# Kernel tuning notes

Measured on AMD Instinct MI355X. Metric: run time of the kernel, lower is better.

Reference implementation:

```python
import jax, jax.numpy as jnp
import numpy as np

D_MODEL = 1024
NUM_HEADS = 16
D_K = D_MODEL // NUM_HEADS


def setup_inputs() -> dict:
    key = jax.random.key(0)
    ks = jax.random.split(key, 9)
    s = 1.0 / np.sqrt(D_MODEL)
    inp = {
        "x": jax.random.normal(ks[0], (4, 2048, D_MODEL), dtype=jnp.float32),
        "W_q": jax.random.uniform(ks[1], (D_MODEL, D_MODEL), jnp.float32, -s, s),
        "b_q": jax.random.uniform(ks[2], (D_MODEL,), jnp.float32, -s, s),
        "W_k": jax.random.uniform(ks[3], (D_MODEL, D_MODEL), jnp.float32, -s, s),
        "b_k": jax.random.uniform(ks[4], (D_MODEL,), jnp.float32, -s, s),
        "W_v": jax.random.uniform(ks[5], (D_MODEL, D_MODEL), jnp.float32, -s, s),
        "b_v": jax.random.uniform(ks[6], (D_MODEL,), jnp.float32, -s, s),
        "W_o": jax.random.uniform(ks[7], (D_MODEL, D_MODEL), jnp.float32, -s, s),
        "b_o": jax.random.uniform(ks[8], (D_MODEL,), jnp.float32, -s, s),
    }
    return inp


def reference(x, W_q, b_q, W_k, b_k, W_v, b_v, W_o, b_o):
    B, S, _ = x.shape
    # Linear layers (torch convention: y = x @ W.T + b), split into heads -> [B, H, S, d_k]
    def proj(W, b):
        y = jnp.einsum("bsd,ed->bse", x, W) + b
        return y.reshape(B, S, NUM_HEADS, D_K).transpose(0, 2, 1, 3)

    Q = proj(W_q, b_q)
    K = proj(W_k, b_k)
    V = proj(W_v, b_v)

    scale = 1.0 / jnp.sqrt(jnp.asarray(D_K, dtype=x.dtype))
    scores = jnp.einsum("bhqd,bhkd->bhqk", Q, K) * scale  # [B, H, S, S]
    attn = jax.nn.softmax(scores, axis=-1)
    out = jnp.einsum("bhqk,bhkd->bhqd", attn, V)  # [B, H, S, d_k]
    out = out.transpose(0, 2, 1, 3).reshape(B, S, D_MODEL)
    return jnp.einsum("bsd,ed->bse", out, W_o) + b_o
```

## Files before the change

kernel.cpp:

```cpp
#include <hip/hip_runtime.h>
#include <math.h>


constexpr int D = 1024;
constexpr int H = 16;
constexpr int DK = 64;

typedef unsigned short u16;
typedef __attribute__((ext_vector_type(8))) short v8s;
typedef __attribute__((ext_vector_type(4))) float v4f;
typedef const __attribute__((address_space(1))) void gvoid;
typedef __attribute__((address_space(3))) void lvoid;

__device__ __forceinline__ u16 rne_bf16(float f) {
  unsigned u = __float_as_uint(f);
  u += 0x7FFFu + ((u >> 16) & 1u);
  return (u16)(u >> 16);
}

__global__ __launch_bounds__(256) void split_kernel(
    const float* __restrict__ in, u16* __restrict__ hi, u16* __restrict__ lo, int n4)
{
  const int i = blockIdx.x * 256 + threadIdx.x;
  if (i >= n4) return;
  const float4 v = ((const float4*)in)[i];
  const float f[4] = {v.x, v.y, v.z, v.w};
  ushort4 h, l;
  u16 hh[4], ll[4];
#pragma unroll
  for (int j = 0; j < 4; ++j) {
    const unsigned u = __float_as_uint(f[j]);
    hh[j] = (u16)(u >> 16);
    const float hf = __uint_as_float(u & 0xFFFF0000u);
    ll[j] = rne_bf16(f[j] - hf);
  }
  h.x = hh[0]; h.y = hh[1]; h.z = hh[2]; h.w = hh[3];
  l.x = ll[0]; l.y = ll[1]; l.z = ll[2]; l.w = ll[3];
  ((ushort4*)hi)[i] = h;
  ((ushort4*)lo)[i] = l;
}

__global__ __launch_bounds__(256) void gemm_mfma_kernel(
    const u16* __restrict__ Ahi, const u16* __restrict__ Alo,
    const u16* __restrict__ Whi, const u16* __restrict__ Wlo,
    const float* __restrict__ bias, void* __restrict__ Cout,
    int M, int S_, int headsplit_in, int out_mode)
{
  __shared__ u16 sAhi[128 * 32];
  __shared__ u16 sAlo[128 * 32];
  __shared__ u16 sBhi[128 * 32];
  __shared__ u16 sBlo[128 * 32];

  const int tid = threadIdx.x;
  const int m0 = blockIdx.x * 128, n0 = blockIdx.y * 128;
  const int lane = tid & 63, w = tid >> 6;
  const int wm = (w >> 1) * 64, wn = (w & 1) * 64;
  const int fr = lane & 15, fq = lane >> 4;

  v4f acc[4][4];
#pragma unroll
  for (int mi = 0; mi < 4; ++mi)
#pragma unroll
    for (int ni = 0; ni < 4; ++ni)
      acc[mi][ni] = (v4f){0.f, 0.f, 0.f, 0.f};

  const int srow = tid >> 2;
  const int skel = (tid & 3) * 8;

  for (int k0 = 0; k0 < D; k0 += 32) {
#pragma unroll
    for (int rep = 0; rep < 2; ++rep) {
      const int row = srow + rep * 64;
      size_t offA;
      if (headsplit_in) {
        const int m = m0 + row;
        const int b = m / S_, s = m - b * S_;
        const int k = k0 + skel;
        const int h = k >> 6, dk = k & 63;
        offA = ((size_t)(b * H + h) * S_ + s) * DK + dk;
      } else {
        offA = (size_t)(m0 + row) * D + k0 + skel;
      }
      const size_t offB = (size_t)(n0 + row) * D + k0 + skel;
      const int ldso = rep * 2048 + tid * 8;
      __builtin_amdgcn_global_load_lds((gvoid*)(Ahi + offA), (lvoid*)(sAhi + ldso), 16, 0, 0);
      __builtin_amdgcn_global_load_lds((gvoid*)(Alo + offA), (lvoid*)(sAlo + ldso), 16, 0, 0);
      __builtin_amdgcn_global_load_lds((gvoid*)(Whi + offB), (lvoid*)(sBhi + ldso), 16, 0, 0);
      __builtin_amdgcn_global_load_lds((gvoid*)(Wlo + offB), (lvoid*)(sBlo + ldso), 16, 0, 0);
    }
    __syncthreads();

    v8s ahi[4], alo[4], bhi[4], blo[4];
#pragma unroll
    for (int t = 0; t < 4; ++t) {
      const int ar = (wm + t * 16 + fr) * 32 + fq * 8;
      const int br = (wn + t * 16 + fr) * 32 + fq * 8;
      ahi[t] = *(const v8s*)&sAhi[ar];
      alo[t] = *(const v8s*)&sAlo[ar];
      bhi[t] = *(const v8s*)&sBhi[br];
      blo[t] = *(const v8s*)&sBlo[br];
    }
#pragma unroll
    for (int mi = 0; mi < 4; ++mi)
#pragma unroll
      for (int ni = 0; ni < 4; ++ni) {
        acc[mi][ni] = __builtin_amdgcn_mfma_f32_16x16x32_bf16(ahi[mi], bhi[ni], acc[mi][ni], 0, 0, 0);
        acc[mi][ni] = __builtin_amdgcn_mfma_f32_16x16x32_bf16(alo[mi], bhi[ni], acc[mi][ni], 0, 0, 0);
        acc[mi][ni] = __builtin_amdgcn_mfma_f32_16x16x32_bf16(ahi[mi], blo[ni], acc[mi][ni], 0, 0, 0);
      }
    __syncthreads();
  }

  float* Cf = (float*)Cout;
  u16* Cb = (u16*)Cout;
#pragma unroll
  for (int mi = 0; mi < 4; ++mi) {
#pragma unroll
    for (int ni = 0; ni < 4; ++ni) {
      const int n = n0 + wn + ni * 16 + fr;
      const float bv = bias[n];
#pragma unroll
      for (int r = 0; r < 4; ++r) {
        const int m = m0 + wm + mi * 16 + fq * 4 + r;
        const float val = acc[mi][ni][r] + bv;
        if (out_mode == 0) {
          Cf[(size_t)m * D + n] = val;
        } else {
          const int b = m / S_, s = m - b * S_;
          const int h = n >> 6, dk = n & 63;
          if (out_mode == 1)
            Cb[((size_t)(b * H + h) * S_ + s) * DK + dk] = rne_bf16(val);
          else
            Cb[((size_t)(b * H + h) * DK + dk) * S_ + s] = rne_bf16(val);
        }
      }
    }
  }
}

__global__ __launch_bounds__(256) void attn_mfma_kernel(
    const u16* __restrict__ Qb, const u16* __restrict__ Kb, const u16* __restrict__ Vtb,
    u16* __restrict__ Ohi, u16* __restrict__ Olo, int S_)
{
  __shared__ u16 Ks[64 * 64];
  __shared__ u16 Vt[64 * 64];
  __shared__ u16 Pl[4][32 * 72];

  const int tid = threadIdx.x;
  const int lane = tid & 63, w = tid >> 6;
  const int fr = lane & 15, fq = lane >> 4;
  const int q0 = blockIdx.x * 128;
  const int wq = w * 32;
  const size_t base = (size_t)(blockIdx.z * H + blockIdx.y) * S_ * DK;

  const int srow = tid >> 3;
  const int scb = (tid & 7) ^ (srow & 7);

  v8s qa[2][2];
#pragma unroll
  for (int mi = 0; mi < 2; ++mi)
#pragma unroll
    for (int ks = 0; ks < 2; ++ks)
      qa[mi][ks] = *(const v8s*)(Qb + base + (size_t)(q0 + wq + mi * 16 + fr) * DK + ks * 32 + fq * 8);

  v4f o[2][4];
  float lsum[2][4];
#pragma unroll
  for (int mi = 0; mi < 2; ++mi) {
#pragma unroll
    for (int ni = 0; ni < 4; ++ni) o[mi][ni] = (v4f){0.f, 0.f, 0.f, 0.f};
#pragma unroll
    for (int r = 0; r < 4; ++r) lsum[mi][r] = 0.f;
  }

  for (int j0 = 0; j0 < S_; j0 += 64) {
    __syncthreads();
#pragma unroll
    for (int rep = 0; rep < 2; ++rep) {
      const int row = rep * 32 + srow;
      const int ldso = rep * 2048 + tid * 8;
      __builtin_amdgcn_global_load_lds((gvoid*)(Kb + base + (size_t)(j0 + row) * DK + scb * 8),
                                       (lvoid*)(Ks + ldso), 16, 0, 0);
      __builtin_amdgcn_global_load_lds((gvoid*)(Vtb + base + (size_t)row * S_ + j0 + scb * 8),
                                       (lvoid*)(Vt + ldso), 16, 0, 0);
    }
    __syncthreads();

    v4f s[2][4];
#pragma unroll
    for (int mi = 0; mi < 2; ++mi)
#pragma unroll
      for (int ni = 0; ni < 4; ++ni) s[mi][ni] = (v4f){0.f, 0.f, 0.f, 0.f};
#pragma unroll
    for (int ks = 0; ks < 2; ++ks) {
      v8s kb[4];
#pragma unroll
      for (int ni = 0; ni < 4; ++ni) {
        const int row = ni * 16 + fr;
        kb[ni] = *(const v8s*)&Ks[row * 64 + (((ks * 4 + fq) ^ (row & 7)) * 8)];
      }
#pragma unroll
      for (int mi = 0; mi < 2; ++mi)
#pragma unroll
        for (int ni = 0; ni < 4; ++ni)
          s[mi][ni] = __builtin_amdgcn_mfma_f32_16x16x32_bf16(qa[mi][ks], kb[ni], s[mi][ni], 0, 0, 0);
    }

#pragma unroll
    for (int mi = 0; mi < 2; ++mi)
#pragma unroll
      for (int ni = 0; ni < 4; ++ni) {
#pragma unroll
        for (int r = 0; r < 4; ++r) {
          const float p = __expf(s[mi][ni][r] * 0.125f);
          s[mi][ni][r] = p;
          lsum[mi][r] += p;
          Pl[w][(mi * 16 + fq * 4 + r) * 72 + ni * 16 + fr] = rne_bf16(p);
        }
      }

#pragma unroll
    for (int ks = 0; ks < 2; ++ks) {
      v8s pa[2], vb[4];
#pragma unroll
      for (int mi = 0; mi < 2; ++mi)
        pa[mi] = *(const v8s*)&Pl[w][(mi * 16 + fr) * 72 + ks * 32 + fq * 8];
#pragma unroll
      for (int ni = 0; ni < 4; ++ni) {
        const int row = ni * 16 + fr;
        vb[ni] = *(const v8s*)&Vt[row * 64 + (((ks * 4 + fq) ^ (row & 7)) * 8)];
      }
#pragma unroll
      for (int mi = 0; mi < 2; ++mi)
#pragma unroll
        for (int ni = 0; ni < 4; ++ni)
          o[mi][ni] = __builtin_amdgcn_mfma_f32_16x16x32_bf16(pa[mi], vb[ni], o[mi][ni], 0, 0, 0);
    }
  }

#pragma unroll
  for (int mi = 0; mi < 2; ++mi)
#pragma unroll
    for (int r = 0; r < 4; ++r) {
#pragma unroll
      for (int off = 1; off < 16; off <<= 1)
        lsum[mi][r] += __shfl_xor(lsum[mi][r], off, 16);
      lsum[mi][r] = 1.f / lsum[mi][r];
    }

#pragma unroll
  for (int mi = 0; mi < 2; ++mi)
#pragma unroll
    for (int ni = 0; ni < 4; ++ni)
#pragma unroll
      for (int r = 0; r < 4; ++r) {
        const float val = o[mi][ni][r] * lsum[mi][r];
        const size_t addr = base + (size_t)(q0 + wq + mi * 16 + fq * 4 + r) * DK + ni * 16 + fr;
        const unsigned u = __float_as_uint(val);
        const u16 hv = (u16)(u >> 16);
        Ohi[addr] = hv;
        Olo[addr] = rne_bf16(val - __uint_as_float(u & 0xFFFF0000u));
      }
}

extern "C" void kernel_launch(void* const* d_in, const int* in_sizes, int n_in,
                              void* d_out, int out_size, void* d_ws, size_t ws_size,
                              hipStream_t stream) {
  const float* x  = (const float*)d_in[0];
  const float* Wq = (const float*)d_in[1];
  const float* bq = (const float*)d_in[2];
  const float* Wk = (const float*)d_in[3];
  const float* bk = (const float*)d_in[4];
  const float* Wv = (const float*)d_in[5];
  const float* bv = (const float*)d_in[6];
  const float* Wo = (const float*)d_in[7];
  const float* bo = (const float*)d_in[8];

  const int M = in_sizes[0] / D;
  const int B = 4;
  const int S_ = M / B;
  const size_t MD = (size_t)M * D;
  const size_t DD = (size_t)D * D;

  u16* Qb    = (u16*)d_ws;
  u16* Kb    = Qb + MD;
  u16* Vtb   = Kb + MD;
  u16* xs_hi = Vtb + MD;
  u16* xs_lo = xs_hi + MD;
  u16* wo_hi = xs_lo + MD;
  u16* wo_lo = wo_hi + DD;

  u16* wq_hi = (u16*)d_out;
  u16* wq_lo = wq_hi + DD;
  u16* wk_hi = wq_lo + DD;
  u16* wk_lo = wk_hi + DD;
  u16* wv_hi = wk_lo + DD;
  u16* wv_lo = wv_hi + DD;

  const int gx = (int)(MD / 4 / 256);
  const int gw = (int)(DD / 4 / 256);

  split_kernel<<<gx, 256, 0, stream>>>(x,  xs_hi, xs_lo, (int)(MD / 4));
  split_kernel<<<gw, 256, 0, stream>>>(Wq, wq_hi, wq_lo, (int)(DD / 4));
  split_kernel<<<gw, 256, 0, stream>>>(Wk, wk_hi, wk_lo, (int)(DD / 4));
  split_kernel<<<gw, 256, 0, stream>>>(Wv, wv_hi, wv_lo, (int)(DD / 4));
  split_kernel<<<gw, 256, 0, stream>>>(Wo, wo_hi, wo_lo, (int)(DD / 4));

  dim3 g(M / 128, D / 128);
  gemm_mfma_kernel<<<g, 256, 0, stream>>>(xs_hi, xs_lo, wq_hi, wq_lo, bq, Qb,  M, S_, 0, 1);
  gemm_mfma_kernel<<<g, 256, 0, stream>>>(xs_hi, xs_lo, wk_hi, wk_lo, bk, Kb,  M, S_, 0, 1);
  gemm_mfma_kernel<<<g, 256, 0, stream>>>(xs_hi, xs_lo, wv_hi, wv_lo, bv, Vtb, M, S_, 0, 2);

  dim3 ga(S_ / 128, H, B);
  attn_mfma_kernel<<<ga, 256, 0, stream>>>(Qb, Kb, Vtb, xs_hi, xs_lo, S_);

  gemm_mfma_kernel<<<g, 256, 0, stream>>>(xs_hi, xs_lo, wo_hi, wo_lo, bo, d_out, M, S_, 1, 0);
}
```

Baseline: 454.6 us.

## Fuse QKV projections into one GEMM launch and transpose attention MFMA layout

Concatenates the split Q/K/V weights into one buffer so a single GEMM launch computes all three projections, selecting bias and output layout per block column. The attention kernel swaps MFMA operand order so each lane holds a query column, which allows packed bf16 stores of P and vectorised output writes. Attention output is written directly in [B,S,D] token-major layout into separate buffers, so the output GEMM no longer needs head-split address math. This trades extra workspace for fewer launches, better tail occupancy and more coalesced stores.

```diff
diff --git a/kernel.cpp b/kernel.cpp
--- a/kernel.cpp
+++ b/kernel.cpp
@@ -1,10 +1,12 @@
 #include <hip/hip_runtime.h>
+#include <hip/hip_bf16.h>
 #include <math.h>
 
 
 constexpr int D = 1024;
 constexpr int H = 16;
 constexpr int DK = 64;
+constexpr int PSTR = 72;
 
 typedef unsigned short u16;
 typedef __attribute__((ext_vector_type(8))) short v8s;
@@ -16,6 +18,11 @@
   unsigned u = __float_as_uint(f);
   u += 0x7FFFu + ((u >> 16) & 1u);
   return (u16)(u >> 16);
+}
+
+__device__ __forceinline__ unsigned pk_bf16(float a, float b) {
+  __hip_bfloat162 t = __float22bfloat162_rn(float2{a, b});
+  return *reinterpret_cast<unsigned*>(&t);
 }
 
 __global__ __launch_bounds__(256) void split_kernel(
@@ -40,30 +47,18 @@
   ((ushort4*)lo)[i] = l;
 }
 
-__global__ __launch_bounds__(256) void gemm_mfma_kernel(
+struct GemmAcc { v4f a[4][4]; };
+
+__device__ __forceinline__ void gemm_body(
     const u16* __restrict__ Ahi, const u16* __restrict__ Alo,
     const u16* __restrict__ Whi, const u16* __restrict__ Wlo,
-    const float* __restrict__ bias, void* __restrict__ Cout,
-    int M, int S_, int headsplit_in, int out_mode)
-{
-  __shared__ u16 sAhi[128 * 32];
-  __shared__ u16 sAlo[128 * 32];
-  __shared__ u16 sBhi[128 * 32];
-  __shared__ u16 sBlo[128 * 32];
-
+    int m0, int nrow0, GemmAcc& g,
+    u16* sAhi, u16* sAlo, u16* sBhi, u16* sBlo)
+{
   const int tid = threadIdx.x;
-  const int m0 = blockIdx.x * 128, n0 = blockIdx.y * 128;
   const int lane = tid & 63, w = tid >> 6;
   const int wm = (w >> 1) * 64, wn = (w & 1) * 64;
   const int fr = lane & 15, fq = lane >> 4;
-
-  v4f acc[4][4];
-#pragma unroll
-  for (int mi = 0; mi < 4; ++mi)
-#pragma unroll
-    for (int ni = 0; ni < 4; ++ni)
-      acc[mi][ni] = (v4f){0.f, 0.f, 0.f, 0.f};
-
   const int srow = tid >> 2;
   const int skel = (tid & 3) * 8;
 
@@ -71,17 +66,8 @@
 #pragma unroll
     for (int rep = 0; rep < 2; ++rep) {
       const int row = srow + rep * 64;
-      size_t offA;
-      if (headsplit_in) {
-        const int m = m0 + row;
-        const int b = m / S_, s = m - b * S_;
-        const int k = k0 + skel;
-        const int h = k >> 6, dk = k & 63;
-        offA = ((size_t)(b * H + h) * S_ + s) * DK + dk;
-      } else {
-        offA = (size_t)(m0 + row) * D + k0 + skel;
-      }
-      const size_t offB = (size_t)(n0 + row) * D + k0 + skel;
+      const size_t offA = (size_t)(m0 + row) * D + k0 + skel;
+      const size_t offB = (size_t)(nrow0 + row) * D + k0 + skel;
       const int ldso = rep * 2048 + tid * 8;
       __builtin_amdgcn_global_load_lds((gvoid*)(Ahi + offA), (lvoid*)(sAhi + ldso), 16, 0, 0);
       __builtin_amdgcn_global_load_lds((gvoid*)(Alo + offA), (lvoid*)(sAlo + ldso), 16, 0, 0);
@@ -104,38 +90,102 @@
     for (int mi = 0; mi < 4; ++mi)
 #pragma unroll
       for (int ni = 0; ni < 4; ++ni) {
-        acc[mi][ni] = __builtin_amdgcn_mfma_f32_16x16x32_bf16(ahi[mi], bhi[ni], acc[mi][ni], 0, 0, 0);
-        acc[mi][ni] = __builtin_amdgcn_mfma_f32_16x16x32_bf16(alo[mi], bhi[ni], acc[mi][ni], 0, 0, 0);
-        acc[mi][ni] = __builtin_amdgcn_mfma_f32_16x16x32_bf16(ahi[mi], blo[ni], acc[mi][ni], 0, 0, 0);
+        g.a[mi][ni] = __builtin_amdgcn_mfma_f32_16x16x32_bf16(ahi[mi], bhi[ni], g.a[mi][ni], 0, 0, 0);
+        g.a[mi][ni] = __builtin_amdgcn_mfma_f32_16x16x32_bf16(alo[mi], bhi[ni], g.a[mi][ni], 0, 0, 0);
+        g.a[mi][ni] = __builtin_amdgcn_mfma_f32_16x16x32_bf16(ahi[mi], blo[ni], g.a[mi][ni], 0, 0, 0);
       }
     __syncthreads();
   }
-
-  float* Cf = (float*)Cout;
-  u16* Cb = (u16*)Cout;
+}
+
+__global__ __launch_bounds__(256) void gemm_qkv_kernel(
+    const u16* __restrict__ Ahi, const u16* __restrict__ Alo,
+    const u16* __restrict__ Whi, const u16* __restrict__ Wlo,
+    const float* __restrict__ bq, const float* __restrict__ bk, const float* __restrict__ bv,
+    u16* __restrict__ Qb, u16* __restrict__ Kb, u16* __restrict__ Vtb,
+    int S_)
+{
+  __shared__ u16 sAhi[128 * 32];
+  __shared__ u16 sAlo[128 * 32];
+  __shared__ u16 sBhi[128 * 32];
+  __shared__ u16 sBlo[128 * 32];
+
+  GemmAcc g;
+#pragma unroll
+  for (int mi = 0; mi < 4; ++mi)
+#pragma unroll
+    for (int ni = 0; ni < 4; ++ni) g.a[mi][ni] = (v4f){0.f, 0.f, 0.f, 0.f};
+
+  const int m0 = blockIdx.x * 128;
+  gemm_body(Ahi, Alo, Whi, Wlo, m0, blockIdx.y * 128, g, sAhi, sAlo, sBhi, sBlo);
+
+  const int wsel = blockIdx.y >> 3;
+  const float* bias = (wsel == 0) ? bq : (wsel == 1) ? bk : bv;
+  u16* Cb = (wsel == 0) ? Qb : (wsel == 1) ? Kb : Vtb;
+  const int n0l = (blockIdx.y & 7) * 128;
+
+  const int tid = threadIdx.x;
+  const int lane = tid & 63, w = tid >> 6;
+  const int wm = (w >> 1) * 64, wn = (w & 1) * 64;
+  const int fr = lane & 15, fq = lane >> 4;
+
 #pragma unroll
   for (int mi = 0; mi < 4; ++mi) {
+#pragma unroll
+    for (int ni = 0; ni < 4; ++ni) {
+      const int n = n0l + wn + ni * 16 + fr;
+      const float bvv = bias[n];
+      const int h = n >> 6, dk = n & 63;
+#pragma unroll
+      for (int r = 0; r < 4; ++r) {
+        const int m = m0 + wm + mi * 16 + fq * 4 + r;
+        const int b = m / S_, s = m - b * S_;
+        const float val = g.a[mi][ni][r] + bvv;
+        if (wsel < 2)
+          Cb[((size_t)(b * H + h) * S_ + s) * DK + dk] = rne_bf16(val);
+        else
+          Cb[((size_t)(b * H + h) * DK + dk) * S_ + s] = rne_bf16(val);
+      }
+    }
+  }
+}
+
+__global__ __launch_bounds__(256) void gemm_out_kernel(
+    const u16* __restrict__ Ahi, const u16* __restrict__ Alo,
+    const u16* __restrict__ Whi, const u16* __restrict__ Wlo,
+    const float* __restrict__ bias, float* __restrict__ C)
+{
+  __shared__ u16 sAhi[128 * 32];
+  __shared__ u16 sAlo[128 * 32];
+  __shared__ u16 sBhi[128 * 32];
+  __shared__ u16 sBlo[128 * 32];
+
+  GemmAcc g;
+#pragma unroll
+  for (int mi = 0; mi < 4; ++mi)
+#pragma unroll
+    for (int ni = 0; ni < 4; ++ni) g.a[mi][ni] = (v4f){0.f, 0.f, 0.f, 0.f};
+
+  const int m0 = blockIdx.x * 128, n0 = blockIdx.y * 128;
+  gemm_body(Ahi, Alo, Whi, Wlo, m0, n0, g, sAhi, sAlo, sBhi, sBlo);
+
+  const int tid = threadIdx.x;
+  const int lane = tid & 63, w = tid >> 6;
+  const int wm = (w >> 1) * 64, wn = (w & 1) * 64;
+  const int fr = lane & 15, fq = lane >> 4;
+
+#pragma unroll
+  for (int mi = 0; mi < 4; ++mi)
 #pragma unroll
     for (int ni = 0; ni < 4; ++ni) {
       const int n = n0 + wn + ni * 16 + fr;
-      const float bv = bias[n];
+      const float bvv = bias[n];
 #pragma unroll
       for (int r = 0; r < 4; ++r) {
         const int m = m0 + wm + mi * 16 + fq * 4 + r;
-        const float val = acc[mi][ni][r] + bv;
-        if (out_mode == 0) {
-          Cf[(size_t)m * D + n] = val;
-        } else {
-          const int b = m / S_, s = m - b * S_;
-          const int h = n >> 6, dk = n & 63;
-          if (out_mode == 1)
-            Cb[((size_t)(b * H + h) * S_ + s) * DK + dk] = rne_bf16(val);
-          else
-            Cb[((size_t)(b * H + h) * DK + dk) * S_ + s] = rne_bf16(val);
-        }
-      }
-    }
-  }
+        C[(size_t)m * D + n] = g.a[mi][ni][r] + bvv;
+      }
+    }
 }
 
 __global__ __launch_bounds__(256) void attn_mfma_kernel(
@@ -144,34 +194,32 @@
 {
   __shared__ u16 Ks[64 * 64];
   __shared__ u16 Vt[64 * 64];
-  __shared__ u16 Pl[4][32 * 72];
+  __shared__ u16 Pl[4][32 * PSTR];
 
   const int tid = threadIdx.x;
   const int lane = tid & 63, w = tid >> 6;
   const int fr = lane & 15, fq = lane >> 4;
   const int q0 = blockIdx.x * 128;
+  const int h = blockIdx.y, b = blockIdx.z;
   const int wq = w * 32;
-  const size_t base = (size_t)(blockIdx.z * H + blockIdx.y) * S_ * DK;
+  const size_t base = (size_t)(b * H + h) * S_ * DK;
 
   const int srow = tid >> 3;
   const int scb = (tid & 7) ^ (srow & 7);
 
   v8s qa[2][2];
 #pragma unroll
-  for (int mi = 0; mi < 2; ++mi)
+  for (int ni = 0; ni < 2; ++ni)
 #pragma unroll
     for (int ks = 0; ks < 2; ++ks)
-      qa[mi][ks] = *(const v8s*)(Qb + base + (size_t)(q0 + wq + mi * 16 + fr) * DK + ks * 32 + fq * 8);
-
-  v4f o[2][4];
-  float lsum[2][4];
-#pragma unroll
-  for (int mi = 0; mi < 2; ++mi) {
-#pragma unroll
-    for (int ni = 0; ni < 4; ++ni) o[mi][ni] = (v4f){0.f, 0.f, 0.f, 0.f};
-#pragma unroll
-    for (int r = 0; r < 4; ++r) lsum[mi][r] = 0.f;
-  }
+      qa[ni][ks] = *(const v8s*)(Qb + base + (size_t)(q0 + wq + ni * 16 + fr) * DK + ks * 32 + fq * 8);
+
+  v4f o[4][2];
+  float lsum[2] = {0.f, 0.f};
+#pragma unroll
+  for (int mi = 0; mi < 4; ++mi)
+#pragma unroll
+    for (int ni = 0; ni < 2; ++ni) o[mi][ni] = (v4f){0.f, 0.f, 0.f, 0.f};
 
   for (int j0 = 0; j0 < S_; j0 += 64) {
     __syncthreads();
@@ -186,81 +234,93 @@
     }
     __syncthreads();
 
-    v4f s[2][4];
-#pragma unroll
-    for (int mi = 0; mi < 2; ++mi)
-#pragma unroll
-      for (int ni = 0; ni < 4; ++ni) s[mi][ni] = (v4f){0.f, 0.f, 0.f, 0.f};
+    v4f s[4][2];
+#pragma unroll
+    for (int mi = 0; mi < 4; ++mi)
+#pragma unroll
+      for (int ni = 0; ni < 2; ++ni) s[mi][ni] = (v4f){0.f, 0.f, 0.f, 0.f};
 #pragma unroll
     for (int ks = 0; ks < 2; ++ks) {
       v8s kb[4];
 #pragma unroll
-      for (int ni = 0; ni < 4; ++ni) {
-        const int row = ni * 16 + fr;
-        kb[ni] = *(const v8s*)&Ks[row * 64 + (((ks * 4 + fq) ^ (row & 7)) * 8)];
-      }
-#pragma unroll
-      for (int mi = 0; mi < 2; ++mi)
-#pragma unroll
-        for (int ni = 0; ni < 4; ++ni)
-          s[mi][ni] = __builtin_amdgcn_mfma_f32_16x16x32_bf16(qa[mi][ks], kb[ni], s[mi][ni], 0, 0, 0);
-    }
-
-#pragma unroll
-    for (int mi = 0; mi < 2; ++mi)
-#pragma unroll
-      for (int ni = 0; ni < 4; ++ni) {
-#pragma unroll
-        for (int r = 0; r < 4; ++r) {
-          const float p = __expf(s[mi][ni][r] * 0.125f);
-          s[mi][ni][r] = p;
-          lsum[mi][r] += p;
-          Pl[w][(mi * 16 + fq * 4 + r) * 72 + ni * 16 + fr] = rne_bf16(p);
-        }
+      for (int mi = 0; mi < 4; ++mi) {
+        const int row = mi * 16 + fr;
+        kb[mi] = *(const v8s*)&Ks[row * 64 + (((ks * 4 + fq) ^ (row & 7)) * 8)];
+      }
+#pragma unroll
+      for (int mi = 0; mi < 4; ++mi)
+#pragma unroll
+        for (int ni = 0; ni < 2; ++ni)
+          s[mi][ni] = __builtin_amdgcn_mfma_f32_16x16x32_bf16(kb[mi], qa[ni][ks], s[mi][ni], 0, 0, 0);
+    }
+
+#pragma unroll
+    for (int mi = 0; mi < 4; ++mi)
+#pragma unroll
+      for (int ni = 0; ni < 2; ++ni) {
+        float p[4];
+#pragma unroll
+        for (int r = 0; r < 4; ++r) p[r] = __expf(s[mi][ni][r] * 0.125f);
+        lsum[ni] += (p[0] + p[1]) + (p[2] + p[3]);
+        uint2 pk;
+        pk.x = pk_bf16(p[0], p[1]);
+        pk.y = pk_bf16(p[2], p[3]);
+        *(uint2*)&Pl[w][(ni * 16 + fr) * PSTR + mi * 16 + fq * 4] = pk;
       }
 
 #pragma unroll
     for (int ks = 0; ks < 2; ++ks) {
-      v8s pa[2], vb[4];
-#pragma unroll
-      for (int mi = 0; mi < 2; ++mi)
-        pa[mi] = *(const v8s*)&Pl[w][(mi * 16 + fr) * 72 + ks * 32 + fq * 8];
-#pragma unroll
-      for (int ni = 0; ni < 4; ++ni) {
-        const int row = ni * 16 + fr;
-        vb[ni] = *(const v8s*)&Vt[row * 64 + (((ks * 4 + fq) ^ (row & 7)) * 8)];
-      }
-#pragma unroll
-      for (int mi = 0; mi < 2; ++mi)
-#pragma unroll
-        for (int ni = 0; ni < 4; ++ni)
-          o[mi][ni] = __builtin_amdgcn_mfma_f32_16x16x32_bf16(pa[mi], vb[ni], o[mi][ni], 0, 0, 0);
-    }
-  }
-
-#pragma unroll
-  for (int mi = 0; mi < 2; ++mi)
-#pragma unroll
-    for (int r = 0; r < 4; ++r) {
-#pragma unroll
-      for (int off = 1; off < 16; off <<= 1)
-        lsum[mi][r] += __shfl_xor(lsum[mi][r], off, 16);
-      lsum[mi][r] = 1.f / lsum[mi][r];
-    }
-
-#pragma unroll
-  for (int mi = 0; mi < 2; ++mi)
-#pragma unroll
-    for (int ni = 0; ni < 4; ++ni)
+      v8s vb[4], pa[2];
+#pragma unroll
+      for (int mi = 0; mi < 4; ++mi) {
+        const int row = mi * 16 + fr;
+        vb[mi] = *(const v8s*)&Vt[row * 64 + (((ks * 4 + fq) ^ (row & 7)) * 8)];
+      }
+#pragma unroll
+      for (int ni = 0; ni < 2; ++ni)
+        pa[ni] = *(const v8s*)&Pl[w][(ni * 16 + fr) * PSTR + ks * 32 + fq * 8];
+#pragma unroll
+      for (int mi = 0; mi < 4; ++mi)
+#pragma unroll
+        for (int ni = 0; ni < 2; ++ni)
+          o[mi][ni] = __builtin_amdgcn_mfma_f32_16x16x32_bf16(vb[mi], pa[ni], o[mi][ni], 0, 0, 0);
+    }
+  }
+
+  float linv[2];
+#pragma unroll
+  for (int ni = 0; ni < 2; ++ni) {
+    float l = lsum[ni];
+    l += __shfl_xor(l, 16);
+    l += __shfl_xor(l, 32);
+    linv[ni] = 1.f / l;
+  }
+
+#pragma unroll
+  for (int ni = 0; ni < 2; ++ni) {
+    const int q = q0 + wq + ni * 16 + fr;
+    const size_t rowbase = (size_t)(b * S_ + q) * D + h * DK;
+#pragma unroll
+    for (int mi = 0; mi < 4; ++mi) {
+      const int d0 = mi * 16 + fq * 4;
+      float v[4];
+      unsigned u[4];
+      float res[4];
 #pragma unroll
       for (int r = 0; r < 4; ++r) {
-        const float val = o[mi][ni][r] * lsum[mi][r];
-        const size_t addr = base + (size_t)(q0 + wq + mi * 16 + fq * 4 + r) * DK + ni * 16 + fr;
-        const unsigned u = __float_as_uint(val);
-        const u16 hv = (u16)(u >> 16);
-        Ohi[addr] = hv;
-        Olo[addr] = rne_bf16(val - __uint_as_float(u & 0xFFFF0000u));
-      }
+        v[r] = o[mi][ni][r] * linv[ni];
+        u[r] = __float_as_uint(v[r]);
+        res[r] = v[r] - __uint_as_float(u[r] & 0xFFFF0000u);
+      }
+      uint2 hi, lo;
+      hi.x = (u[1] & 0xFFFF0000u) | (u[0] >> 16);
+      hi.y = (u[3] & 0xFFFF0000u) | (u[2] >> 16);
+      lo.x = pk_bf16(res[0], res[1]);
+      lo.y = pk_bf16(res[2], res[3]);
+      *(uint2*)(Ohi + rowbase + d0) = hi;
+      *(uint2*)(Olo + rowbase + d0) = lo;
+    }
+  }
 }
 
 extern "C" void kernel_launch(void* const* d_in, const int* in_sizes, int n_in,
@@ -287,32 +347,30 @@
   u16* Vtb   = Kb + MD;
   u16* xs_hi = Vtb + MD;
   u16* xs_lo = xs_hi + MD;
-  u16* wo_hi = xs_lo + MD;
+  u16* Ohi   = xs_lo + MD;
+  u16* Olo   = Ohi + MD;
+  u16* wo_hi = Olo + MD;
   u16* wo_lo = wo_hi + DD;
 
-  u16* wq_hi = (u16*)d_out;
-  u16* wq_lo = wq_hi + DD;
-  u16* wk_hi = wq_lo + DD;
-  u16* wk_lo = wk_hi + DD;
-  u16* wv_hi = wk_lo + DD;
-  u16* wv_lo = wv_hi + DD;
+  u16* wqkv_hi = (u16*)d_out;
+  u16* wqkv_lo = wqkv_hi + 3 * DD;
 
   const int gx = (int)(MD / 4 / 256);
   const int gw = (int)(DD / 4 / 256);
 
   split_kernel<<<gx, 256, 0, stream>>>(x,  xs_hi, xs_lo, (int)(MD / 4));
-  split_kernel<<<gw, 256, 0, stream>>>(Wq, wq_hi, wq_lo, (int)(DD / 4));
-  split_kernel<<<gw, 256, 0, stream>>>(Wk, wk_hi, wk_lo, (int)(DD / 4));
-  split_kernel<<<gw, 256, 0, stream>>>(Wv, wv_hi, wv_lo, (int)(DD / 4));
+  split_kernel<<<gw, 256, 0, stream>>>(Wq, wqkv_hi,          wqkv_lo,          (int)(DD / 4));
+  split_kernel<<<gw, 256, 0, stream>>>(Wk, wqkv_hi + DD,     wqkv_lo + DD,     (int)(DD / 4));
+  split_kernel<<<gw, 256, 0, stream>>>(Wv, wqkv_hi + 2 * DD, wqkv_lo + 2 * DD, (int)(DD / 4));
   split_kernel<<<gw, 256, 0, stream>>>(Wo, wo_hi, wo_lo, (int)(DD / 4));
 
-  dim3 g(M / 128, D / 128);
-  gemm_mfma_kernel<<<g, 256, 0, stream>>>(xs_hi, xs_lo, wq_hi, wq_lo, bq, Qb,  M, S_, 0, 1);
-  gemm_mfma_kernel<<<g, 256, 0, stream>>>(xs_hi, xs_lo, wk_hi, wk_lo, bk, Kb,  M, S_, 0, 1);
-  gemm_mfma_kernel<<<g, 256, 0, stream>>>(xs_hi, xs_lo, wv_hi, wv_lo, bv, Vtb, M, S_, 0, 2);
+  dim3 gq(M / 128, 3 * D / 128);
+  gemm_qkv_kernel<<<gq, 256, 0, stream>>>(xs_hi, xs_lo, wqkv_hi, wqkv_lo,
+                                          bq, bk, bv, Qb, Kb, Vtb, S_);
 
   dim3 ga(S_ / 128, H, B);
-  attn_mfma_kernel<<<ga, 256, 0, stream>>>(Qb, Kb, Vtb, xs_hi, xs_lo, S_);
-
-  gemm_mfma_kernel<<<g, 256, 0, stream>>>(xs_hi, xs_lo, wo_hi, wo_lo, bo, d_out, M, S_, 1, 0);
-}
+  attn_mfma_kernel<<<ga, 256, 0, stream>>>(Qb, Kb, Vtb, Ohi, Olo, S_);
+
+  dim3 go(M / 128, D / 128);
+  gemm_out_kernel<<<go, 256, 0, stream>>>(Ohi, Olo, wo_hi, wo_lo, bo, (float*)d_out);
+}
```

After: 441.6 us. 2.9% less time.
